# Performance work log

Measured on AMD Instinct MI355X. Metric: run time of the kernel, lower is better.

Reference implementation:

```python
import jax, jax.numpy as jnp
import numpy as np


def setup_inputs() -> dict:
    key = jax.random.key(0)
    k1, k2 = jax.random.split(key)
    n, h, L, d = 4, 16, 1024, 64
    max_positions = 512
    query = jax.random.normal(k1, (n, h, L, d), dtype=jnp.float32)
    rel_emb = jax.random.normal(k2, (h, d, 2 * max_positions + 1), dtype=jnp.float32)
    return {"query": query, "rel_emb": rel_emb, "length": L}


def reference(query, rel_emb, length):
    # logits: [n, h, i, 2*max_positions+1]
    logits = jnp.einsum('nhid,hdj->nhij', query, rel_emb)
    max_positions = (rel_emb.shape[-1] - 1) // 2
    idx = jnp.arange(length)
    # relative offsets grid [i, j] = j - i  (last=False path)
    grid = idx[None, :] - idx[:, None]
    # clamp to valid range and shift to table indices
    table_idx = jnp.clip(grid, 1 - max_positions, max_positions - 1) + max_positions
    n, h = logits.shape[0], logits.shape[1]
    gather_idx = jnp.broadcast_to(table_idx[None, None, :, :], (n, h, length, length))
    # out[n,h,i,j] = logits[n,h,i,table_idx[i,j]]
    out = jnp.take_along_axis(logits, gather_idx, axis=-1)
    return out
```

## Files before the change

kernel.cpp:

```cpp
#include <hip/hip_runtime.h>
#include <hip/hip_bf16.h>


#define NH 16
#define LQ 1024
#define DD 64
#define TT 1025
#define MAXP 512
#define PADS 4
#define LSTRIDE2 1036

typedef float f32x4 __attribute__((ext_vector_type(4)));
typedef short s16x4 __attribute__((ext_vector_type(4)));
typedef short s16x8 __attribute__((ext_vector_type(8)));

__device__ __forceinline__ short f2bf(float f) {
    __hip_bfloat16 h = __float2bfloat16(f);
    return __builtin_bit_cast(short, h);
}
__device__ __forceinline__ float bf2f(short s) {
    return __builtin_bit_cast(float, ((unsigned)(unsigned short)s) << 16);
}

template<int D>
__device__ __forceinline__ void write_chunks(const unsigned short* __restrict__ lrow,
                                             float p1, float p2,
                                             int i, int l, float* __restrict__ orow) {
    #pragma unroll
    for (int c = 0; c < 4; ++c) {
        const int j0 = c * 256 + 4 * l;
        const int t0 = j0 - i + MAXP;
        int colA = PADS + t0 - D;
        colA = colA < 0 ? 0 : (colA > PADS + LQ ? PADS + LQ : colA);
        s16x4 A = *(const s16x4*)(lrow + colA);
        s16x4 B = {0, 0, 0, 0};
        if (D) B = *(const s16x4*)(lrow + colA + 4);
        f32x4 v;
        #pragma unroll
        for (int e = 0; e < 4; ++e) {
            const int t = t0 + e;
            const float in = bf2f((D + e < 4) ? A[D + e] : B[D + e - 4]);
            v[e] = t < 1 ? p1 : (t > LQ - 1 ? p2 : in);
        }
        __builtin_nontemporal_store(v, (f32x4*)(orow + j0));
    }
}

__global__ __launch_bounds__(256, 4) void lpb_fused(const float* __restrict__ Q,
                                                    const float* __restrict__ R,
                                                    float* __restrict__ out) {
    __shared__ unsigned short lg[16][LSTRIDE2];

    const int ib  = blockIdx.x;
    const int nh  = blockIdx.y;
    const int h   = nh & (NH - 1);
    const int tid = threadIdx.x;
    const int w   = tid >> 6, l = tid & 63;
    const int n   = l & 15, g = l >> 4;
    const int ibase = ib * 16;

    const float* qrow = Q + ((size_t)nh * LQ + (ibase + n)) * DD + 8 * g;
    s16x8 qf[2];
    #pragma unroll
    for (int kh = 0; kh < 2; ++kh) {
        f32x4 a = *(const f32x4*)(qrow + kh * 32);
        f32x4 b = *(const f32x4*)(qrow + kh * 32 + 4);
        #pragma unroll
        for (int r = 0; r < 4; ++r) { qf[kh][r] = f2bf(a[r]); qf[kh][4 + r] = f2bf(b[r]); }
    }

    const float* rbase = R + (size_t)(h * DD + 8 * g) * TT;
    #pragma unroll 4
    for (int mt = 0; mt < 16; ++mt) {
        const int tb = w * 256 + mt * 16;
        const float* rc = rbase + tb + n;
        s16x8 rf0, rf1;
        #pragma unroll
        for (int r = 0; r < 8; ++r) {
            rf0[r] = f2bf(rc[(size_t)r * TT]);
            rf1[r] = f2bf(rc[(size_t)(32 + r) * TT]);
        }
        f32x4 acc = (f32x4){0.f, 0.f, 0.f, 0.f};
        acc = __builtin_amdgcn_mfma_f32_16x16x32_bf16(rf0, qf[0], acc, 0, 0, 0);
        acc = __builtin_amdgcn_mfma_f32_16x16x32_bf16(rf1, qf[1], acc, 0, 0, 0);
        s16x4 hv;
        #pragma unroll
        for (int s = 0; s < 4; ++s) hv[s] = f2bf(acc[s]);
        *(s16x4*)&lg[n][PADS + tb + 4 * g] = hv;
    }
    __syncthreads();

    #pragma unroll
    for (int rr = 0; rr < 4; ++rr) {
        const int il = 4 * w + rr;
        const int i  = ibase + il;
        const unsigned short* lrow = &lg[il][0];
        const float p1 = bf2f(lrow[PADS + 1]);
        const float p2 = bf2f(lrow[PADS + LQ - 1]);
        float* orow = out + ((size_t)nh * LQ + i) * LQ;
        switch ((MAXP - i) & 3) {
            case 0: write_chunks<0>(lrow, p1, p2, i, l, orow); break;
            case 1: write_chunks<1>(lrow, p1, p2, i, l, orow); break;
            case 2: write_chunks<2>(lrow, p1, p2, i, l, orow); break;
            default: write_chunks<3>(lrow, p1, p2, i, l, orow); break;
        }
    }
}

extern "C" void kernel_launch(void* const* d_in, const int* in_sizes, int n_in,
                              void* d_out, int out_size, void* d_ws, size_t ws_size,
                              hipStream_t stream) {
    const float* Q = (const float*)d_in[0];
    const float* R = (const float*)d_in[1];
    float* out = (float*)d_out;

    lpb_fused<<<dim3(64, 64), 256, 0, stream>>>(Q, R, out);
}
```

Before: 80.69 us.

## Stream logits through per-wave LDS ring buffers, interleaving MFMA compute with output writes

Each wave now owns 16 query rows and computes the logit tiles it needs incrementally into a 288-entry ring buffer in LDS. It writes each 256-column output chunk as soon as the required logits exist, which removes the block-wide barrier and the full 1024-wide logit table. The grid is flattened with a swizzled block index so blocks sharing a head are spread out, and each block now covers 64 rows instead of 16. This overlaps computation with the store-bound output stream and shrinks LDS use, in exchange for modular ring indexing and more serialized per-wave work.

```diff
diff --git a/kernel.cpp b/kernel.cpp
--- a/kernel.cpp
+++ b/kernel.cpp
@@ -7,8 +7,8 @@
 #define DD 64
 #define TT 1025
 #define MAXP 512
-#define PADS 4
-#define LSTRIDE2 1036
+#define RING 288
+#define RSTRIDE 296
 
 typedef float f32x4 __attribute__((ext_vector_type(4)));
 typedef short s16x4 __attribute__((ext_vector_type(4)));
@@ -18,48 +18,54 @@
     __hip_bfloat16 h = __float2bfloat16(f);
     return __builtin_bit_cast(short, h);
 }
-__device__ __forceinline__ float bf2f(short s) {
-    return __builtin_bit_cast(float, ((unsigned)(unsigned short)s) << 16);
+__device__ __forceinline__ float bf2f(unsigned short s) {
+    return __builtin_bit_cast(float, ((unsigned)s) << 16);
+}
+__device__ __forceinline__ int mod288(int x) {
+    return x >= 864 ? x - 864 : (x >= 576 ? x - 576 : (x >= 288 ? x - 288 : x));
 }
 
 template<int D>
-__device__ __forceinline__ void write_chunks(const unsigned short* __restrict__ lrow,
-                                             float p1, float p2,
-                                             int i, int l, float* __restrict__ orow) {
+__device__ __forceinline__ void write_row(const unsigned short* __restrict__ lrow,
+                                          int i, int c, int l,
+                                          float* __restrict__ orow) {
+    const float p1 = bf2f(lrow[1]);
+    const float p2 = bf2f(lrow[159]);
+    const int j0 = c * 256 + 4 * l;
+    const int t0 = j0 - i + MAXP;
+    const int tA = t0 - D;
+    int a = tA;     a = a < 0 ? 0 : (a > 1020 ? 1020 : a);
+    int b = tA + 4; b = b < 0 ? 0 : (b > 1020 ? 1020 : b);
+    const s16x4 A = *(const s16x4*)(lrow + mod288(a));
+    const s16x4 B = *(const s16x4*)(lrow + mod288(b));
+    f32x4 v;
     #pragma unroll
-    for (int c = 0; c < 4; ++c) {
-        const int j0 = c * 256 + 4 * l;
-        const int t0 = j0 - i + MAXP;
-        int colA = PADS + t0 - D;
-        colA = colA < 0 ? 0 : (colA > PADS + LQ ? PADS + LQ : colA);
-        s16x4 A = *(const s16x4*)(lrow + colA);
-        s16x4 B = {0, 0, 0, 0};
-        if (D) B = *(const s16x4*)(lrow + colA + 4);
-        f32x4 v;
-        #pragma unroll
-        for (int e = 0; e < 4; ++e) {
-            const int t = t0 + e;
-            const float in = bf2f((D + e < 4) ? A[D + e] : B[D + e - 4]);
-            v[e] = t < 1 ? p1 : (t > LQ - 1 ? p2 : in);
-        }
-        __builtin_nontemporal_store(v, (f32x4*)(orow + j0));
+    for (int e = 0; e < 4; ++e) {
+        const int t = t0 + e;
+        const short in = (D + e < 4) ? A[D + e] : B[D + e - 4];
+        v[e] = t < 1 ? p1 : (t > LQ - 1 ? p2 : bf2f((unsigned short)in));
     }
+    __builtin_nontemporal_store(v, (f32x4*)(orow + j0));
 }
 
-__global__ __launch_bounds__(256, 4) void lpb_fused(const float* __restrict__ Q,
-                                                    const float* __restrict__ R,
-                                                    float* __restrict__ out) {
-    __shared__ unsigned short lg[16][LSTRIDE2];
+__global__ __launch_bounds__(256, 4) void lpb_stream(const float* __restrict__ Q,
+                                                     const float* __restrict__ R,
+                                                     float* __restrict__ out) {
+    __shared__ unsigned short lg[4][16][RSTRIDE];
 
-    const int ib  = blockIdx.x;
-    const int nh  = blockIdx.y;
-    const int h   = nh & (NH - 1);
+    const int bidx = blockIdx.x;
+    const int swz  = (bidx & 7) * 128 + (bidx >> 3);
+    const int nh   = swz >> 4;
+    const int rg   = swz & 15;
+    const int h    = nh & (NH - 1);
+
     const int tid = threadIdx.x;
-    const int w   = tid >> 6, l = tid & 63;
-    const int n   = l & 15, g = l >> 4;
-    const int ibase = ib * 16;
+    const int w = tid >> 6, l = tid & 63;
+    const int n = l & 15, g = l >> 4;
+    const int base = rg * 64 + w * 16;
+    unsigned short (*ring)[RSTRIDE] = lg[w];
 
-    const float* qrow = Q + ((size_t)nh * LQ + (ibase + n)) * DD + 8 * g;
+    const float* qrow = Q + ((size_t)nh * LQ + (base + n)) * DD + 8 * g;
     s16x8 qf[2];
     #pragma unroll
     for (int kh = 0; kh < 2; ++kh) {
@@ -70,39 +76,47 @@
     }
 
     const float* rbase = R + (size_t)(h * DD + 8 * g) * TT;
-    #pragma unroll 4
-    for (int mt = 0; mt < 16; ++mt) {
-        const int tb = w * 256 + mt * 16;
-        const float* rc = rbase + tb + n;
-        s16x8 rf0, rf1;
-        #pragma unroll
-        for (int r = 0; r < 8; ++r) {
-            rf0[r] = f2bf(rc[(size_t)r * TT]);
-            rf1[r] = f2bf(rc[(size_t)(32 + r) * TT]);
+    float* obase = out + (size_t)nh * LQ * LQ;
+
+    int computed = 0;
+    int ringc = 0;
+
+    #pragma unroll 1
+    for (int c = 0; c < 4; ++c) {
+        const int Thi = 256 * c + 767 - base;
+        int need = (Thi + 16) >> 4;
+        need = need < 1 ? 1 : (need > 64 ? 64 : need);
+
+        #pragma unroll 1
+        for (; computed < need; ++computed) {
+            const int tb = computed << 4;
+            const float* rc = rbase + tb + n;
+            s16x8 rf0, rf1;
+            #pragma unroll
+            for (int r = 0; r < 8; ++r) {
+                rf0[r] = f2bf(rc[(size_t)r * TT]);
+                rf1[r] = f2bf(rc[(size_t)(32 + r) * TT]);
+            }
+            f32x4 acc = (f32x4){0.f, 0.f, 0.f, 0.f};
+            acc = __builtin_amdgcn_mfma_f32_16x16x32_bf16(rf0, qf[0], acc, 0, 0, 0);
+            acc = __builtin_amdgcn_mfma_f32_16x16x32_bf16(rf1, qf[1], acc, 0, 0, 0);
+            s16x4 hv;
+            #pragma unroll
+            for (int s = 0; s < 4; ++s) hv[s] = f2bf(acc[s]);
+            *(s16x4*)&ring[n][ringc + 4 * g] = hv;
+            ringc += 16; if (ringc == RING) ringc = 0;
         }
-        f32x4 acc = (f32x4){0.f, 0.f, 0.f, 0.f};
-        acc = __builtin_amdgcn_mfma_f32_16x16x32_bf16(rf0, qf[0], acc, 0, 0, 0);
-        acc = __builtin_amdgcn_mfma_f32_16x16x32_bf16(rf1, qf[1], acc, 0, 0, 0);
-        s16x4 hv;
-        #pragma unroll
-        for (int s = 0; s < 4; ++s) hv[s] = f2bf(acc[s]);
-        *(s16x4*)&lg[n][PADS + tb + 4 * g] = hv;
-    }
-    __syncthreads();
 
-    #pragma unroll
-    for (int rr = 0; rr < 4; ++rr) {
-        const int il = 4 * w + rr;
-        const int i  = ibase + il;
-        const unsigned short* lrow = &lg[il][0];
-        const float p1 = bf2f(lrow[PADS + 1]);
-        const float p2 = bf2f(lrow[PADS + LQ - 1]);
-        float* orow = out + ((size_t)nh * LQ + i) * LQ;
-        switch ((MAXP - i) & 3) {
-            case 0: write_chunks<0>(lrow, p1, p2, i, l, orow); break;
-            case 1: write_chunks<1>(lrow, p1, p2, i, l, orow); break;
-            case 2: write_chunks<2>(lrow, p1, p2, i, l, orow); break;
-            default: write_chunks<3>(lrow, p1, p2, i, l, orow); break;
+        #pragma unroll 1
+        for (int q = 0; q < 4; ++q) {
+            { const int rr = ((2048 + MAXP - base - 0) & 3) + 4 * q; const int i = base + rr;
+              write_row<0>(&ring[rr][0], i, c, l, obase + (size_t)i * LQ); }
+            { const int rr = ((2048 + MAXP - base - 1) & 3) + 4 * q; const int i = base + rr;
+              write_row<1>(&ring[rr][0], i, c, l, obase + (size_t)i * LQ); }
+            { const int rr = ((2048 + MAXP - base - 2) & 3) + 4 * q; const int i = base + rr;
+              write_row<2>(&ring[rr][0], i, c, l, obase + (size_t)i * LQ); }
+            { const int rr = ((2048 + MAXP - base - 3) & 3) + 4 * q; const int i = base + rr;
+              write_row<3>(&ring[rr][0], i, c, l, obase + (size_t)i * LQ); }
         }
     }
 }
@@ -114,5 +128,5 @@
     const float* R = (const float*)d_in[1];
     float* out = (float*)d_out;
 
-    lpb_fused<<<dim3(64, 64), 256, 0, stream>>>(Q, R, out);
+    lpb_stream<<<dim3(1024), 256, 0, stream>>>(Q, R, out);
 }
```

Result: slower. 84.05 us (+4.2%).

## Split block into producer and consumer waves with double-buffered LDS

Applied to the files above, without the earlier changes.

Converts the kernel into a persistent-style producer/consumer design. Two waves compute bf16 MFMA logits for the next 16-row unit into one LDS buffer while two waves stream the gathered output rows for the previous unit from the other buffer. Each block now handles 8 units, and a swizzled 1D grid maps blocks to (n,h) groups. The aim is to overlap the GEMM with the store-bound output write. The cost is half as many waves doing each phase, a barrier per round, and lower occupancy from the doubled LDS and the reduced launch bounds.

```diff
diff --git a/kernel.cpp b/kernel.cpp
--- a/kernel.cpp
+++ b/kernel.cpp
@@ -9,6 +9,7 @@
 #define MAXP 512
 #define PADS 4
 #define LSTRIDE2 1036
+#define UNITS 8
 
 typedef float f32x4 __attribute__((ext_vector_type(4)));
 typedef short s16x4 __attribute__((ext_vector_type(4)));
@@ -46,64 +47,81 @@
     }
 }
 
-__global__ __launch_bounds__(256, 4) void lpb_fused(const float* __restrict__ Q,
-                                                    const float* __restrict__ R,
-                                                    float* __restrict__ out) {
-    __shared__ unsigned short lg[16][LSTRIDE2];
+__global__ __launch_bounds__(256, 2) void lpb_pc(const float* __restrict__ Q,
+                                                 const float* __restrict__ R,
+                                                 float* __restrict__ out) {
+    __shared__ unsigned short lg[2][16][LSTRIDE2];
 
-    const int ib  = blockIdx.x;
-    const int nh  = blockIdx.y;
-    const int h   = nh & (NH - 1);
+    const int bidx = blockIdx.x;
+    const int swz  = (bidx & 7) * 64 + (bidx >> 3);
+    const int nh   = swz >> 3;
+    const int ibg  = swz & 7;
+    const int h    = nh & (NH - 1);
+
     const int tid = threadIdx.x;
-    const int w   = tid >> 6, l = tid & 63;
-    const int n   = l & 15, g = l >> 4;
-    const int ibase = ib * 16;
-
-    const float* qrow = Q + ((size_t)nh * LQ + (ibase + n)) * DD + 8 * g;
-    s16x8 qf[2];
-    #pragma unroll
-    for (int kh = 0; kh < 2; ++kh) {
-        f32x4 a = *(const f32x4*)(qrow + kh * 32);
-        f32x4 b = *(const f32x4*)(qrow + kh * 32 + 4);
-        #pragma unroll
-        for (int r = 0; r < 4; ++r) { qf[kh][r] = f2bf(a[r]); qf[kh][4 + r] = f2bf(b[r]); }
-    }
+    const int w = tid >> 6, l = tid & 63;
+    const int n = l & 15, g = l >> 4;
 
     const float* rbase = R + (size_t)(h * DD + 8 * g) * TT;
-    #pragma unroll 4
-    for (int mt = 0; mt < 16; ++mt) {
-        const int tb = w * 256 + mt * 16;
-        const float* rc = rbase + tb + n;
-        s16x8 rf0, rf1;
-        #pragma unroll
-        for (int r = 0; r < 8; ++r) {
-            rf0[r] = f2bf(rc[(size_t)r * TT]);
-            rf1[r] = f2bf(rc[(size_t)(32 + r) * TT]);
+
+    #pragma unroll 1
+    for (int rnd = 0; rnd <= UNITS; ++rnd) {
+        if (w < 2) {
+            if (rnd < UNITS) {
+                const int ibase = (ibg * UNITS + rnd) * 16;
+                const float* qrow = Q + ((size_t)nh * LQ + (ibase + n)) * DD + 8 * g;
+                s16x8 qf[2];
+                #pragma unroll
+                for (int kh = 0; kh < 2; ++kh) {
+                    f32x4 a = *(const f32x4*)(qrow + kh * 32);
+                    f32x4 b = *(const f32x4*)(qrow + kh * 32 + 4);
+                    #pragma unroll
+                    for (int e = 0; e < 4; ++e) { qf[kh][e] = f2bf(a[e]); qf[kh][4 + e] = f2bf(b[e]); }
+                }
+                unsigned short (*buf)[LSTRIDE2] = lg[rnd & 1];
+                #pragma unroll 4
+                for (int mt = 0; mt < 32; ++mt) {
+                    const int tb = w * 512 + mt * 16;
+                    const float* rc = rbase + tb + n;
+                    s16x8 rf0, rf1;
+                    #pragma unroll
+                    for (int e = 0; e < 8; ++e) {
+                        rf0[e] = f2bf(rc[(size_t)e * TT]);
+                        rf1[e] = f2bf(rc[(size_t)(32 + e) * TT]);
+                    }
+                    f32x4 acc = (f32x4){0.f, 0.f, 0.f, 0.f};
+                    acc = __builtin_amdgcn_mfma_f32_16x16x32_bf16(rf0, qf[0], acc, 0, 0, 0);
+                    acc = __builtin_amdgcn_mfma_f32_16x16x32_bf16(rf1, qf[1], acc, 0, 0, 0);
+                    s16x4 hv;
+                    #pragma unroll
+                    for (int s = 0; s < 4; ++s) hv[s] = f2bf(acc[s]);
+                    *(s16x4*)&buf[n][PADS + tb + 4 * g] = hv;
+                }
+            }
+        } else {
+            if (rnd > 0) {
+                const int u = rnd - 1;
+                const int ibase = (ibg * UNITS + u) * 16;
+                unsigned short (*buf)[LSTRIDE2] = lg[u & 1];
+                const int cw = w - 2;
+                #pragma unroll 1
+                for (int rr = 0; rr < 8; ++rr) {
+                    const int il = cw * 8 + rr;
+                    const int i  = ibase + il;
+                    const unsigned short* lrow = &buf[il][0];
+                    const float p1 = bf2f(lrow[PADS + 1]);
+                    const float p2 = bf2f(lrow[PADS + LQ - 1]);
+                    float* orow = out + ((size_t)nh * LQ + i) * LQ;
+                    switch ((MAXP - i) & 3) {
+                        case 0: write_chunks<0>(lrow, p1, p2, i, l, orow); break;
+                        case 1: write_chunks<1>(lrow, p1, p2, i, l, orow); break;
+                        case 2: write_chunks<2>(lrow, p1, p2, i, l, orow); break;
+                        default: write_chunks<3>(lrow, p1, p2, i, l, orow); break;
+                    }
+                }
+            }
         }
-        f32x4 acc = (f32x4){0.f, 0.f, 0.f, 0.f};
-        acc = __builtin_amdgcn_mfma_f32_16x16x32_bf16(rf0, qf[0], acc, 0, 0, 0);
-        acc = __builtin_amdgcn_mfma_f32_16x16x32_bf16(rf1, qf[1], acc, 0, 0, 0);
-        s16x4 hv;
-        #pragma unroll
-        for (int s = 0; s < 4; ++s) hv[s] = f2bf(acc[s]);
-        *(s16x4*)&lg[n][PADS + tb + 4 * g] = hv;
-    }
-    __syncthreads();
-
-    #pragma unroll
-    for (int rr = 0; rr < 4; ++rr) {
-        const int il = 4 * w + rr;
-        const int i  = ibase + il;
-        const unsigned short* lrow = &lg[il][0];
-        const float p1 = bf2f(lrow[PADS + 1]);
-        const float p2 = bf2f(lrow[PADS + LQ - 1]);
-        float* orow = out + ((size_t)nh * LQ + i) * LQ;
-        switch ((MAXP - i) & 3) {
-            case 0: write_chunks<0>(lrow, p1, p2, i, l, orow); break;
-            case 1: write_chunks<1>(lrow, p1, p2, i, l, orow); break;
-            case 2: write_chunks<2>(lrow, p1, p2, i, l, orow); break;
-            default: write_chunks<3>(lrow, p1, p2, i, l, orow); break;
-        }
+        __syncthreads();
     }
 }
 
@@ -114,5 +132,5 @@
     const float* R = (const float*)d_in[1];
     float* out = (float*)d_out;
 
-    lpb_fused<<<dim3(64, 64), 256, 0, stream>>>(Q, R, out);
+    lpb_pc<<<dim3(512), 256, 0, stream>>>(Q, R, out);
 }
```

New measurement: 74.19 us (median of 2 runs). 8.1% less time.
